# Performance work log

Hardware: AMD Instinct MI355X
Metric: run time of the kernel (lower is better)

The kernel has to match this reference:

```python
import jax, jax.numpy as jnp
import numpy as np

EPS = 1e-8  # torch nn.CosineSimilarity default eps


def setup_inputs() -> dict:
    key = jax.random.key(0)
    k1, k2 = jax.random.split(key)
    query = jax.random.normal(k1, (8, 2048, 64), dtype=jnp.float32)
    y = jax.random.normal(k2, (8, 2048, 64), dtype=jnp.float32)
    return {"query": query, "y": y}


def _l2_normalize(x):
    # x / max(||x||, eps) along last dim (matches torch cosine_similarity clamping)
    n = jnp.sqrt(jnp.sum(x * x, axis=-1, keepdims=True))
    return x / jnp.maximum(n, EPS)


def reference(query, y):
    # Algebraically equivalent to broadcast CosineSimilarity over [B,Lq,Ly,D]:
    # normalize once, then batched GEMM -> [B, Lq, Ly]
    qn = _l2_normalize(query)          # [B, Lq, D]
    yn = _l2_normalize(y)              # [B, Ly, D]
    att = jnp.einsum("bqd,bkd->bqk", qn, yn)  # [B, Lq, Ly]
    sim = jnp.max(att, axis=2)[:, None, :]     # [B, 1, Lq]
    return (att, sim)
```

## Files before the change

### kernel.cpp

```cpp
#include <hip/hip_runtime.h>

#define LL 2048
#define DD 64
#define BB 8
#define EPSF 1e-8f

#define NELEM ((size_t)BB * LL * DD)

typedef short bf16x8 __attribute__((ext_vector_type(8)));
typedef float f32x4 __attribute__((ext_vector_type(4)));
typedef float f32x8 __attribute__((ext_vector_type(8)));

__device__ __forceinline__ ushort f2bf(float f) {
    uint u = __float_as_uint(f);
    return (ushort)((u + 0x7fffu + ((u >> 16) & 1u)) >> 16);
}
__device__ __forceinline__ float bf2f(ushort h) {
    return __uint_as_float((uint)h << 16);
}

__global__ __launch_bounds__(256) void norm_y_kernel(
    const float* __restrict__ y, ushort* __restrict__ yh) {
    const int row = blockIdx.x * 32 + (threadIdx.x >> 3);
    const int oct = threadIdx.x & 7;
    const float* g = y + (size_t)row * DD;
    float4 v0 = *reinterpret_cast<const float4*>(g + oct * 4);
    float4 v1 = *reinterpret_cast<const float4*>(g + 32 + oct * 4);
    float ss = v0.x*v0.x + v0.y*v0.y + v0.z*v0.z + v0.w*v0.w
             + v1.x*v1.x + v1.y*v1.y + v1.z*v1.z + v1.w*v1.w;
    ss += __shfl_xor(ss, 1);
    ss += __shfl_xor(ss, 2);
    ss += __shfl_xor(ss, 4);
    const float sc = 1.0f / fmaxf(sqrtf(ss), EPSF);
    const size_t base = (size_t)row * DD + oct * 4;
    *reinterpret_cast<ushort4*>(yh + base) =
        make_ushort4(f2bf(v0.x*sc), f2bf(v0.y*sc), f2bf(v0.z*sc), f2bf(v0.w*sc));
    *reinterpret_cast<ushort4*>(yh + base + 32) =
        make_ushort4(f2bf(v1.x*sc), f2bf(v1.y*sc), f2bf(v1.z*sc), f2bf(v1.w*sc));
}

__global__ __launch_bounds__(256, 3) void att_mfma_kernel(
    const float* __restrict__ q, const ushort* __restrict__ yhg,
    float* __restrict__ out) {
    const int b       = blockIdx.y;
    const int rowBase = blockIdx.x * 32;
    const int t  = threadIdx.x;
    const int w  = t >> 6;
    const int l  = t & 63;
    const int ln = l & 15;
    const int kg = l >> 4;

    bf16x8 qhf[2][2], qlf[2][2];
    #pragma unroll
    for (int mq = 0; mq < 2; ++mq) {
        f32x8 v[2];
        #pragma unroll
        for (int kk = 0; kk < 2; ++kk)
            v[kk] = *reinterpret_cast<const f32x8*>(
                q + ((size_t)(b * LL + rowBase + mq * 16 + ln)) * DD + kk * 32 + kg * 8);
        float ss = 0.f;
        #pragma unroll
        for (int kk = 0; kk < 2; ++kk)
            #pragma unroll
            for (int j = 0; j < 8; ++j) ss += v[kk][j] * v[kk][j];
        ss += __shfl_xor(ss, 16);
        ss += __shfl_xor(ss, 32);
        const float sc = 1.0f / fmaxf(sqrtf(ss), EPSF);
        #pragma unroll
        for (int kk = 0; kk < 2; ++kk)
            #pragma unroll
            for (int j = 0; j < 8; ++j) {
                const float f = v[kk][j] * sc;
                const ushort h = f2bf(f);
                qhf[mq][kk][j] = (short)h;
                qlf[mq][kk][j] = (short)f2bf(f - bf2f(h));
            }
    }

    float rmax[2] = {-1e30f, -1e30f};

    bf16x8 yh0[4][2], yh1[4][2];

#define LOADY(DH, CT) do {                                                       \
    const int colBase_ = (CT) * 256 + w * 64;                                    \
    _Pragma("unroll")                                                            \
    for (int ny = 0; ny < 4; ++ny)                                               \
        _Pragma("unroll")                                                        \
        for (int kk = 0; kk < 2; ++kk)                                           \
            DH[ny][kk] = *reinterpret_cast<const bf16x8*>(                       \
                yhg + ((size_t)(b * LL + colBase_ + ny * 16 + ln)) * DD          \
                    + kk * 32 + kg * 8);                                         \
} while (0)

#define COMPSTORE(SH, CT) do {                                                   \
    const int colBase_ = (CT) * 256 + w * 64;                                    \
    f32x4 acc[2][4];                                                             \
    _Pragma("unroll")                                                            \
    for (int mq = 0; mq < 2; ++mq)                                               \
        _Pragma("unroll")                                                        \
        for (int ny = 0; ny < 4; ++ny)                                           \
            acc[mq][ny] = (f32x4){0.f, 0.f, 0.f, 0.f};                           \
    _Pragma("unroll")                                                            \
    for (int kk = 0; kk < 2; ++kk)                                               \
        _Pragma("unroll")                                                        \
        for (int mq = 0; mq < 2; ++mq)                                           \
            _Pragma("unroll")                                                    \
            for (int ny = 0; ny < 4; ++ny)                                       \
                acc[mq][ny] = __builtin_amdgcn_mfma_f32_16x16x32_bf16(           \
                    SH[ny][kk], qlf[mq][kk], acc[mq][ny], 0, 0, 0);              \
    _Pragma("unroll")                                                            \
    for (int kk = 0; kk < 2; ++kk)                                               \
        _Pragma("unroll")                                                        \
        for (int mq = 0; mq < 2; ++mq)                                           \
            _Pragma("unroll")                                                    \
            for (int ny = 0; ny < 4; ++ny)                                       \
                acc[mq][ny] = __builtin_amdgcn_mfma_f32_16x16x32_bf16(           \
                    SH[ny][kk], qhf[mq][kk], acc[mq][ny], 0, 0, 0);              \
    _Pragma("unroll")                                                            \
    for (int mq = 0; mq < 2; ++mq) {                                             \
        _Pragma("unroll")                                                        \
        for (int ny = 0; ny < 4; ++ny) {                                         \
            f32x4 v = acc[mq][ny];                                               \
            *reinterpret_cast<f32x4*>(                                           \
                out + ((size_t)(b * LL + rowBase + mq * 16 + ln)) * LL           \
                    + colBase_ + ny * 16 + kg * 4) = v;                          \
            rmax[mq] = fmaxf(rmax[mq],                                           \
                       fmaxf(fmaxf(v[0], v[1]), fmaxf(v[2], v[3])));             \
        }                                                                        \
    }                                                                            \
} while (0)

    LOADY(yh0, 0);
    #pragma unroll
    for (int ct = 0; ct < 8; ct += 2) {
        if (ct + 1 < 8) LOADY(yh1, ct + 1);
        COMPSTORE(yh0, ct);
        if (ct + 2 < 8) LOADY(yh0, ct + 2);
        if (ct + 1 < 8) COMPSTORE(yh1, ct + 1);
    }

    #pragma unroll
    for (int mq = 0; mq < 2; ++mq) {
        rmax[mq] = fmaxf(rmax[mq], __shfl_xor(rmax[mq], 16));
        rmax[mq] = fmaxf(rmax[mq], __shfl_xor(rmax[mq], 32));
    }

    __shared__ float smax[4][32];
    if (kg == 0) {
        smax[w][ln]      = rmax[0];
        smax[w][16 + ln] = rmax[1];
    }
    __syncthreads();
    if (t < 32) {
        const float v = fmaxf(fmaxf(smax[0][t], smax[1][t]),
                              fmaxf(smax[2][t], smax[3][t]));
        out[(size_t)BB * LL * LL + (size_t)b * LL + rowBase + t] = v;
    }
#undef LOADY
#undef COMPSTORE
}

extern "C" void kernel_launch(void* const* d_in, const int* in_sizes, int n_in,
                              void* d_out, int out_size, void* d_ws, size_t ws_size,
                              hipStream_t stream) {
    const float* q = (const float*)d_in[0];
    const float* y = (const float*)d_in[1];
    float* out     = (float*)d_out;
    ushort* yh     = (ushort*)d_ws;

    norm_y_kernel<<<dim3(512), dim3(256), 0, stream>>>(y, yh);
    att_mfma_kernel<<<dim3(LL / 32, BB), dim3(256), 0, stream>>>(q, yh, out);
}
```

Baseline: 150.4 us.

## Use 512-thread blocks and drop manual Y double-buffering in attention kernel

Doubles the block to 8 waves, so each wave covers a 512-column stride and runs 4 column tiles instead of 8. The explicit register double-buffer of Y fragments is removed in favour of a simple load-then-compute loop. This lowers register pressure and raises the waves per CU available to hide latency, but gives up explicit software prefetch of the next tile. The shared-memory max reduction is widened to 8 waves to match.

```diff
diff --git a/kernel.cpp b/kernel.cpp
--- a/kernel.cpp
+++ b/kernel.cpp
@@ -4,8 +4,6 @@
 #define DD 64
 #define BB 8
 #define EPSF 1e-8f
-
-#define NELEM ((size_t)BB * LL * DD)
 
 typedef short bf16x8 __attribute__((ext_vector_type(8)));
 typedef float f32x4 __attribute__((ext_vector_type(4)));
@@ -39,7 +37,7 @@
         make_ushort4(f2bf(v1.x*sc), f2bf(v1.y*sc), f2bf(v1.z*sc), f2bf(v1.w*sc));
 }
 
-__global__ __launch_bounds__(256, 3) void att_mfma_kernel(
+__global__ __launch_bounds__(512, 4) void att_mfma_kernel(
     const float* __restrict__ q, const ushort* __restrict__ yhg,
     float* __restrict__ out) {
     const int b       = blockIdx.y;
@@ -79,64 +77,53 @@
 
     float rmax[2] = {-1e30f, -1e30f};
 
-    bf16x8 yh0[4][2], yh1[4][2];
+    for (int ct = 0; ct < 4; ++ct) {
+        const int colBase = ct * 512 + w * 64;
 
-#define LOADY(DH, CT) do {                                                       \
-    const int colBase_ = (CT) * 256 + w * 64;                                    \
-    _Pragma("unroll")                                                            \
-    for (int ny = 0; ny < 4; ++ny)                                               \
-        _Pragma("unroll")                                                        \
-        for (int kk = 0; kk < 2; ++kk)                                           \
-            DH[ny][kk] = *reinterpret_cast<const bf16x8*>(                       \
-                yhg + ((size_t)(b * LL + colBase_ + ny * 16 + ln)) * DD          \
-                    + kk * 32 + kg * 8);                                         \
-} while (0)
+        bf16x8 yh[4][2];
+        #pragma unroll
+        for (int ny = 0; ny < 4; ++ny)
+            #pragma unroll
+            for (int kk = 0; kk < 2; ++kk)
+                yh[ny][kk] = *reinterpret_cast<const bf16x8*>(
+                    yhg + ((size_t)(b * LL + colBase + ny * 16 + ln)) * DD
+                        + kk * 32 + kg * 8);
 
-#define COMPSTORE(SH, CT) do {                                                   \
-    const int colBase_ = (CT) * 256 + w * 64;                                    \
-    f32x4 acc[2][4];                                                             \
-    _Pragma("unroll")                                                            \
-    for (int mq = 0; mq < 2; ++mq)                                               \
-        _Pragma("unroll")                                                        \
-        for (int ny = 0; ny < 4; ++ny)                                           \
-            acc[mq][ny] = (f32x4){0.f, 0.f, 0.f, 0.f};                           \
-    _Pragma("unroll")                                                            \
-    for (int kk = 0; kk < 2; ++kk)                                               \
-        _Pragma("unroll")                                                        \
-        for (int mq = 0; mq < 2; ++mq)                                           \
-            _Pragma("unroll")                                                    \
-            for (int ny = 0; ny < 4; ++ny)                                       \
-                acc[mq][ny] = __builtin_amdgcn_mfma_f32_16x16x32_bf16(           \
-                    SH[ny][kk], qlf[mq][kk], acc[mq][ny], 0, 0, 0);              \
-    _Pragma("unroll")                                                            \
-    for (int kk = 0; kk < 2; ++kk)                                               \
-        _Pragma("unroll")                                                        \
-        for (int mq = 0; mq < 2; ++mq)                                           \
-            _Pragma("unroll")                                                    \
-            for (int ny = 0; ny < 4; ++ny)                                       \
-                acc[mq][ny] = __builtin_amdgcn_mfma_f32_16x16x32_bf16(           \
-                    SH[ny][kk], qhf[mq][kk], acc[mq][ny], 0, 0, 0);              \
-    _Pragma("unroll")                                                            \
-    for (int mq = 0; mq < 2; ++mq) {                                             \
-        _Pragma("unroll")                                                        \
-        for (int ny = 0; ny < 4; ++ny) {                                         \
-            f32x4 v = acc[mq][ny];                                               \
-            *reinterpret_cast<f32x4*>(                                           \
-                out + ((size_t)(b * LL + rowBase + mq * 16 + ln)) * LL           \
-                    + colBase_ + ny * 16 + kg * 4) = v;                          \
-            rmax[mq] = fmaxf(rmax[mq],                                           \
-                       fmaxf(fmaxf(v[0], v[1]), fmaxf(v[2], v[3])));             \
-        }                                                                        \
-    }                                                                            \
-} while (0)
+        f32x4 acc[2][4];
+        #pragma unroll
+        for (int mq = 0; mq < 2; ++mq)
+            #pragma unroll
+            for (int ny = 0; ny < 4; ++ny)
+                acc[mq][ny] = (f32x4){0.f, 0.f, 0.f, 0.f};
 
-    LOADY(yh0, 0);
-    #pragma unroll
-    for (int ct = 0; ct < 8; ct += 2) {
-        if (ct + 1 < 8) LOADY(yh1, ct + 1);
-        COMPSTORE(yh0, ct);
-        if (ct + 2 < 8) LOADY(yh0, ct + 2);
-        if (ct + 1 < 8) COMPSTORE(yh1, ct + 1);
+        #pragma unroll
+        for (int kk = 0; kk < 2; ++kk)
+            #pragma unroll
+            for (int mq = 0; mq < 2; ++mq)
+                #pragma unroll
+                for (int ny = 0; ny < 4; ++ny)
+                    acc[mq][ny] = __builtin_amdgcn_mfma_f32_16x16x32_bf16(
+                        yh[ny][kk], qlf[mq][kk], acc[mq][ny], 0, 0, 0);
+        #pragma unroll
+        for (int kk = 0; kk < 2; ++kk)
+            #pragma unroll
+            for (int mq = 0; mq < 2; ++mq)
+                #pragma unroll
+                for (int ny = 0; ny < 4; ++ny)
+                    acc[mq][ny] = __builtin_amdgcn_mfma_f32_16x16x32_bf16(
+                        yh[ny][kk], qhf[mq][kk], acc[mq][ny], 0, 0, 0);
+
+        #pragma unroll
+        for (int mq = 0; mq < 2; ++mq)
+            #pragma unroll
+            for (int ny = 0; ny < 4; ++ny) {
+                f32x4 v = acc[mq][ny];
+                *reinterpret_cast<f32x4*>(
+                    out + ((size_t)(b * LL + rowBase + mq * 16 + ln)) * LL
+                        + colBase + ny * 16 + kg * 4) = v;
+                rmax[mq] = fmaxf(rmax[mq],
+                           fmaxf(fmaxf(v[0], v[1]), fmaxf(v[2], v[3])));
+            }
     }
 
     #pragma unroll
@@ -145,19 +132,18 @@
         rmax[mq] = fmaxf(rmax[mq], __shfl_xor(rmax[mq], 32));
     }
 
-    __shared__ float smax[4][32];
+    __shared__ float smax[8][32];
     if (kg == 0) {
         smax[w][ln]      = rmax[0];
         smax[w][16 + ln] = rmax[1];
     }
     __syncthreads();
     if (t < 32) {
-        const float v = fmaxf(fmaxf(smax[0][t], smax[1][t]),
-                              fmaxf(smax[2][t], smax[3][t]));
+        float v = smax[0][t];
+        #pragma unroll
+        for (int ww = 1; ww < 8; ++ww) v = fmaxf(v, smax[ww][t]);
         out[(size_t)BB * LL * LL + (size_t)b * LL + rowBase + t] = v;
     }
-#undef LOADY
-#undef COMPSTORE
 }
 
 extern "C" void kernel_launch(void* const* d_in, const int* in_sizes, int n_in,
@@ -169,5 +155,5 @@
     ushort* yh     = (ushort*)d_ws;
 
     norm_y_kernel<<<dim3(512), dim3(256), 0, stream>>>(y, yh);
-    att_mfma_kernel<<<dim3(LL / 32, BB), dim3(256), 0, stream>>>(q, yh, out);
+    att_mfma_kernel<<<dim3(LL / 32, BB), dim3(512), 0, stream>>>(q, yh, out);
 }
```

Result: slower. 155.6 us (+3.5%).

## Use 512-thread blocks with 8 waves and deeper Y prefetch pipeline

Applied to the files above, without the earlier changes.

Doubles the block size to 8 waves so each wave covers 64 columns of a 512-column tile. Each wave now makes 4 tile passes instead of 8, with a four-buffer software pipeline. Accumulator stores are split from the MFMA compute so loads for the next tiles issue earlier. This aims to raise memory-level parallelism and hide store and load latency, at the cost of more registers per wave and a higher occupancy target that may force spills.

```diff
diff --git a/kernel.cpp b/kernel.cpp
--- a/kernel.cpp
+++ b/kernel.cpp
@@ -4,8 +4,6 @@
 #define DD 64
 #define BB 8
 #define EPSF 1e-8f
-
-#define NELEM ((size_t)BB * LL * DD)
 
 typedef short bf16x8 __attribute__((ext_vector_type(8)));
 typedef float f32x4 __attribute__((ext_vector_type(4)));
@@ -39,7 +37,7 @@
         make_ushort4(f2bf(v1.x*sc), f2bf(v1.y*sc), f2bf(v1.z*sc), f2bf(v1.w*sc));
 }
 
-__global__ __launch_bounds__(256, 3) void att_mfma_kernel(
+__global__ __launch_bounds__(512, 4) void att_mfma_kernel(
     const float* __restrict__ q, const ushort* __restrict__ yhg,
     float* __restrict__ out) {
     const int b       = blockIdx.y;
@@ -78,23 +76,21 @@
     }
 
     float rmax[2] = {-1e30f, -1e30f};
+    f32x4 acc[2][4];
+    bf16x8 yA[4][2], yB[4][2], yC[4][2], yD[4][2];
 
-    bf16x8 yh0[4][2], yh1[4][2];
-
-#define LOADY(DH, CT) do {                                                       \
-    const int colBase_ = (CT) * 256 + w * 64;                                    \
+#define LOADY(BUF, CT) do {                                                      \
+    const int colBase_ = (CT) * 512 + w * 64;                                    \
     _Pragma("unroll")                                                            \
     for (int ny = 0; ny < 4; ++ny)                                               \
         _Pragma("unroll")                                                        \
         for (int kk = 0; kk < 2; ++kk)                                           \
-            DH[ny][kk] = *reinterpret_cast<const bf16x8*>(                       \
+            BUF[ny][kk] = *reinterpret_cast<const bf16x8*>(                      \
                 yhg + ((size_t)(b * LL + colBase_ + ny * 16 + ln)) * DD          \
                     + kk * 32 + kg * 8);                                         \
 } while (0)
 
-#define COMPSTORE(SH, CT) do {                                                   \
-    const int colBase_ = (CT) * 256 + w * 64;                                    \
-    f32x4 acc[2][4];                                                             \
+#define COMP(BUF) do {                                                           \
     _Pragma("unroll")                                                            \
     for (int mq = 0; mq < 2; ++mq)                                               \
         _Pragma("unroll")                                                        \
@@ -107,7 +103,7 @@
             _Pragma("unroll")                                                    \
             for (int ny = 0; ny < 4; ++ny)                                       \
                 acc[mq][ny] = __builtin_amdgcn_mfma_f32_16x16x32_bf16(           \
-                    SH[ny][kk], qlf[mq][kk], acc[mq][ny], 0, 0, 0);              \
+                    BUF[ny][kk], qlf[mq][kk], acc[mq][ny], 0, 0, 0);             \
     _Pragma("unroll")                                                            \
     for (int kk = 0; kk < 2; ++kk)                                               \
         _Pragma("unroll")                                                        \
@@ -115,9 +111,13 @@
             _Pragma("unroll")                                                    \
             for (int ny = 0; ny < 4; ++ny)                                       \
                 acc[mq][ny] = __builtin_amdgcn_mfma_f32_16x16x32_bf16(           \
-                    SH[ny][kk], qhf[mq][kk], acc[mq][ny], 0, 0, 0);              \
+                    BUF[ny][kk], qhf[mq][kk], acc[mq][ny], 0, 0, 0);             \
+} while (0)
+
+#define STOREACC(CT) do {                                                        \
+    const int colBase_ = (CT) * 512 + w * 64;                                    \
     _Pragma("unroll")                                                            \
-    for (int mq = 0; mq < 2; ++mq) {                                             \
+    for (int mq = 0; mq < 2; ++mq)                                               \
         _Pragma("unroll")                                                        \
         for (int ny = 0; ny < 4; ++ny) {                                         \
             f32x4 v = acc[mq][ny];                                               \
@@ -127,17 +127,24 @@
             rmax[mq] = fmaxf(rmax[mq],                                           \
                        fmaxf(fmaxf(v[0], v[1]), fmaxf(v[2], v[3])));             \
         }                                                                        \
-    }                                                                            \
 } while (0)
 
-    LOADY(yh0, 0);
-    #pragma unroll
-    for (int ct = 0; ct < 8; ct += 2) {
-        if (ct + 1 < 8) LOADY(yh1, ct + 1);
-        COMPSTORE(yh0, ct);
-        if (ct + 2 < 8) LOADY(yh0, ct + 2);
-        if (ct + 1 < 8) COMPSTORE(yh1, ct + 1);
-    }
+    LOADY(yA, 0);
+    LOADY(yB, 1);
+    COMP(yA);
+    LOADY(yC, 2);
+    STOREACC(0);
+    COMP(yB);
+    LOADY(yD, 3);
+    STOREACC(1);
+    COMP(yC);
+    STOREACC(2);
+    COMP(yD);
+    STOREACC(3);
+
+#undef LOADY
+#undef COMP
+#undef STOREACC
 
     #pragma unroll
     for (int mq = 0; mq < 2; ++mq) {
@@ -145,19 +152,18 @@
         rmax[mq] = fmaxf(rmax[mq], __shfl_xor(rmax[mq], 32));
     }
 
-    __shared__ float smax[4][32];
+    __shared__ float smax[8][32];
     if (kg == 0) {
         smax[w][ln]      = rmax[0];
         smax[w][16 + ln] = rmax[1];
     }
     __syncthreads();
     if (t < 32) {
-        const float v = fmaxf(fmaxf(smax[0][t], smax[1][t]),
-                              fmaxf(smax[2][t], smax[3][t]));
+        float v = smax[0][t];
+        #pragma unroll
+        for (int ww = 1; ww < 8; ++ww) v = fmaxf(v, smax[ww][t]);
         out[(size_t)BB * LL * LL + (size_t)b * LL + rowBase + t] = v;
     }
-#undef LOADY
-#undef COMPSTORE
 }
 
 extern "C" void kernel_launch(void* const* d_in, const int* in_sizes, int n_in,
@@ -169,5 +175,5 @@
     ushort* yh     = (ushort*)d_ws;
 
     norm_y_kernel<<<dim3(512), dim3(256), 0, stream>>>(y, yh);
-    att_mfma_kernel<<<dim3(LL / 32, BB), dim3(256), 0, stream>>>(q, yh, out);
+    att_mfma_kernel<<<dim3(LL / 32, BB), dim3(512), 0, stream>>>(q, yh, out);
 }
```

New measurement: 187.6 us. 1.25x slower.
